# Kernel optimization log

Measured on AMD Instinct MI355X. Metric: run time of the kernel, lower is better.

## Reference

```python
import jax, jax.numpy as jnp
import numpy as np

T, B, E, H = 2048, 2, 1024, 16
D = E // H
MAX_REL = 16  # RelativePosition default max_relative_position


def setup_inputs() -> dict:
    key = jax.random.key(0)
    ks = jax.random.split(key, 11)
    s = 1.0 / np.sqrt(E)
    inp = {
        'query': jax.random.normal(ks[0], (T, B, E), dtype=jnp.float32),
        'Wq': jax.random.normal(ks[1], (E, E), dtype=jnp.float32) * s,
        'bq': jnp.zeros((E,), dtype=jnp.float32),
        'Wk': jax.random.normal(ks[2], (E, E), dtype=jnp.float32) * s,
        'bk': jnp.zeros((E,), dtype=jnp.float32),
        'Wv': jax.random.normal(ks[3], (E, E), dtype=jnp.float32) * s,
        'bv': jnp.zeros((E,), dtype=jnp.float32),
        'Wo': jax.random.normal(ks[4], (E, E), dtype=jnp.float32) * s,
        'bo': jnp.zeros((E,), dtype=jnp.float32),
        'rk_table': jax.random.normal(ks[5], (2 * MAX_REL + 1, D), dtype=jnp.float32) * 0.05,
        'rv_table': jax.random.normal(ks[6], (2 * MAX_REL + 1, D), dtype=jnp.float32) * 0.05,
    }
    return inp


def _rel_idx(lq, lk):
    # distance_mat = k - q, clipped to [-MAX_REL, MAX_REL], shifted to [0, 2*MAX_REL]
    d = jnp.arange(lk)[None, :] - jnp.arange(lq)[:, None]
    return jnp.clip(d, -MAX_REL, MAX_REL) + MAX_REL  # [lq, lk] int


def reference(query, Wq, bq, Wk, bk, Wv, bv, Wo, bo, rk_table, rv_table):
    t, b, e = query.shape
    scale = D ** -0.5
    # projections (torch Linear: x @ W.T + b)
    q = (query @ Wq.T + bq) * scale
    k = query @ Wk.T + bk
    v = query @ Wv.T + bv
    # [T,B,E] -> [B*H, T, D]
    q = q.reshape(t, b * H, D).transpose(1, 0, 2)
    k = k.reshape(t, b * H, D).transpose(1, 0, 2)
    v = v.reshape(t, b * H, D).transpose(1, 0, 2)
    # content scores + Shaw relative-position key scores
    scores = jnp.einsum('ntd,nsd->nts', q, k)            # [N, T, S]
    rk = rk_table[_rel_idx(t, t)]                        # [T, S, D]
    scores = scores + jnp.einsum('ntd,tsd->nts', q, rk)  # relpos_k term
    probs = jax.nn.softmax(scores, axis=-1)
    # weighted values + Shaw relative-position value term
    rv = rv_table[_rel_idx(t, t)]                        # [T, S, D]
    attn = jnp.einsum('nts,nsd->ntd', probs, v) + jnp.einsum('nts,tsd->ntd', probs, rv)
    # [B*H, T, D] -> [T, B, E]
    attn = attn.transpose(1, 0, 2).reshape(t, b, e)
    return attn @ Wo.T + bo
```

## Files before the change

kernel.cpp:

```cpp
#include <hip/hip_runtime.h>
#include <hip/hip_bf16.h>
#include <math.h>

#define T_   2048
#define B_   2
#define E_   1024
#define H_   16
#define D_   64
#define NH_  32
#define M_   4096

typedef __attribute__((ext_vector_type(8))) short s8b;
typedef __attribute__((ext_vector_type(4))) float f4;

#define MFMA_B16(a,b,c) __builtin_amdgcn_mfma_f32_16x16x32_bf16(a,b,c,0,0,0)
#define LOG2E 1.44269504088896f

__device__ __forceinline__ unsigned short f2bu(float f) {
    union { __hip_bfloat16 h; unsigned short u; } cv;
    cv.h = __float2bfloat16(f);
    return cv.u;
}
__device__ __forceinline__ unsigned short f2bu_fast(float f) {
    return (unsigned short)((__float_as_uint(f) + 0x8000u) >> 16);
}
__device__ __forceinline__ float bu2f(unsigned short u) {
    union { __hip_bfloat16 h; unsigned short u; } cv; cv.u = u;
    return __bfloat162float(cv.h);
}
__device__ __forceinline__ unsigned int pk2(float a, float b) {
    return (unsigned int)f2bu(a) | ((unsigned int)f2bu(b) << 16);
}
__device__ __forceinline__ unsigned int pk2_fast(float a, float b) {
    return ((__float_as_uint(a) + 0x8000u) >> 16) |
           ((__float_as_uint(b) + 0x8000u) & 0xFFFF0000u);
}
__device__ __forceinline__ float fexp2(float x) {
    return __builtin_amdgcn_exp2f(x);
}
__device__ __forceinline__ float ld1d(const void* p, size_t idx, bool f32) {
    return f32 ? ((const float*)p)[idx] : bu2f(((const unsigned short*)p)[idx]);
}
__device__ __forceinline__ float qsumq(float v) {
    v += __shfl_xor(v, 16); v += __shfl_xor(v, 32);
    return v;
}
__device__ __forceinline__ void glds16(const unsigned short* g, unsigned short* l) {
    __builtin_amdgcn_global_load_lds(
        (const __attribute__((address_space(1))) unsigned int*)g,
        (__attribute__((address_space(3))) unsigned int*)l, 16, 0, 0);
}

__global__ void detect_dtype(const unsigned short* __restrict__ q, int* __restrict__ flag) {
    int e = (q[threadIdx.x] >> 7) & 0xFF;
    bool sane = (e == 0) || (e >= 97 && e <= 157);
    unsigned long long m = __ballot(sane);
    if (threadIdx.x == 0) *flag = (__popcll(m) >= 56) ? 0 : 1;
}

__global__ __launch_bounds__(256) void cvt_bf16(
    const void* __restrict__ x,
    const void* __restrict__ Wq, const void* __restrict__ Wk,
    const void* __restrict__ Wv, const void* __restrict__ Wo,
    const void* __restrict__ bq, const void* __restrict__ bk,
    const void* __restrict__ bv, const void* __restrict__ bo,
    unsigned short* __restrict__ xw, unsigned short* __restrict__ Ww,
    unsigned short* __restrict__ bw, const int* __restrict__ flag)
{
    const bool f32m = (*flag != 0);
    const int y = blockIdx.y;
    const void* src; unsigned short* dst; int n;
    if (y == 0)      { src = x; dst = xw; n = M_ * E_; }
    else if (y <= 4) {
        src = (y == 1) ? Wq : (y == 2) ? Wk : (y == 3) ? Wv : Wo;
        dst = Ww + (size_t)(y - 1) * E_ * E_; n = E_ * E_;
    } else {
        src = (y == 5) ? bq : (y == 6) ? bk : (y == 7) ? bv : bo;
        dst = bw + (size_t)(y - 5) * E_; n = E_;
    }
    int i = (blockIdx.x * 256 + threadIdx.x) * 8;
    if (i >= n) return;
    if (f32m) {
        const float* s = (const float*)src + i;
        float4 f0 = *(const float4*)s, f1 = *(const float4*)(s + 4);
        union { unsigned int d[4]; s8b v; } u;
        u.d[0] = pk2(f0.x, f0.y); u.d[1] = pk2(f0.z, f0.w);
        u.d[2] = pk2(f1.x, f1.y); u.d[3] = pk2(f1.z, f1.w);
        *(s8b*)(dst + i) = u.v;
    } else {
        *(s8b*)(dst + i) = *(const s8b*)((const unsigned short*)src + i);
    }
}

__global__ __launch_bounds__(256, 3) void qkv_gemm(
    const unsigned short* __restrict__ xw, const unsigned short* __restrict__ Ww,
    const unsigned short* __restrict__ bw,
    unsigned short* __restrict__ qo, unsigned short* __restrict__ ko,
    unsigned short* __restrict__ vo)
{
    const int bid = blockIdx.x;
    const int r_ = bid & 7, s_ = bid >> 3;
    const int g = r_ + 8 * (s_ >> 3);
    const int e0 = (s_ & 7) * 128;
    const int m0 = (g & 31) * 128;
    const int p  = g >> 5;
    const unsigned short* W    = Ww + (size_t)p * E_ * E_;
    const unsigned short* bias = bw + (size_t)p * E_;
    const float scale = (p == 0) ? 0.125f * LOG2E : 1.0f;

    const int tid = threadIdx.x, w = tid >> 6, lane = tid & 63;
    const int quad = lane >> 4, lc = lane & 15;
    const int wx = w & 1, wy = w >> 1;

    __shared__ unsigned short a_s[2][128 * 32];
    __shared__ unsigned short b_s[2][128 * 32];

    f4 acc[4][4];
    #pragma unroll
    for (int i = 0; i < 4; i++)
        #pragma unroll
        for (int j = 0; j < 4; j++) acc[i][j] = (f4){0.f, 0.f, 0.f, 0.f};

    const int gr = lane >> 2;
    const int gc = (lane & 3) ^ ((lane >> 2) & 3);
    const size_t aoff = (size_t)(m0 + w*32 + gr) * E_ + gc*8;
    const size_t boff = (size_t)(e0 + w*32 + gr) * E_ + gc*8;

    #pragma unroll
    for (int j = 0; j < 2; j++) {
        glds16(xw + aoff + (size_t)j*16*E_, &a_s[0][(w*128 + j*64) * 8]);
        glds16(W  + boff + (size_t)j*16*E_, &b_s[0][(w*128 + j*64) * 8]);
    }
    __syncthreads();

    const int fcA = quad ^ (lc & 3);
    for (int k0 = 0; k0 < E_; k0 += 32) {
        const int cur = (k0 >> 5) & 1;
        if (k0 + 32 < E_) {
            #pragma unroll
            for (int j = 0; j < 2; j++) {
                glds16(xw + aoff + (size_t)j*16*E_ + k0 + 32, &a_s[cur^1][(w*128 + j*64) * 8]);
                glds16(W  + boff + (size_t)j*16*E_ + k0 + 32, &b_s[cur^1][(w*128 + j*64) * 8]);
            }
        }
        s8b af[4], bfr[4];
        #pragma unroll
        for (int i = 0; i < 4; i++)
            af[i]  = *(const s8b*)&a_s[cur][((wy*64 + i*16 + lc)*4 + fcA) * 8];
        #pragma unroll
        for (int i = 0; i < 4; i++)
            bfr[i] = *(const s8b*)&b_s[cur][((wx*64 + i*16 + lc)*4 + fcA) * 8];
        #pragma unroll
        for (int ms = 0; ms < 4; ms++)
            #pragma unroll
            for (int ns = 0; ns < 4; ns++)
                acc[ms][ns] = MFMA_B16(af[ms], bfr[ns], acc[ms][ns]);
        __syncthreads();
    }

    float bias_v[4];
    #pragma unroll
    for (int ns = 0; ns < 4; ns++) bias_v[ns] = bu2f(bias[e0 + wx*64 + ns*16 + lc]);

    if (p < 2) {
        #pragma unroll
        for (int ms = 0; ms < 4; ms++)
            #pragma unroll
            for (int ns = 0; ns < 4; ns++)
                #pragma unroll
                for (int r2 = 0; r2 < 4; r2++) {
                    float val = (acc[ms][ns][r2] + bias_v[ns]) * scale;
                    float nb = __shfl_xor(val, 1);
                    if (!(lane & 1)) {
                        int m = m0 + wy*64 + ms*16 + quad*4 + r2;
                        int t = m >> 1, bb = m & 1;
                        int e = e0 + wx*64 + ns*16 + lc;
                        int h = e >> 6, d = e & 63;
                        unsigned short* dst = (p == 0) ? qo : ko;
                        *(unsigned int*)&dst[(((size_t)(bb*H_ + h) * T_ + t) << 6) + d] = pk2(val, nb);
                    }
                }
    } else {
        #pragma unroll
        for (int ms = 0; ms < 4; ms++) {
            int t0v = (m0 + wy*64 + ms*16 + quad*4) >> 1;
            #pragma unroll
            for (int ns = 0; ns < 4; ns++) {
                int e = e0 + wx*64 + ns*16 + lc;
                int h = e >> 6, d = e & 63;
                float v0 = acc[ms][ns][0] + bias_v[ns];
                float v1 = acc[ms][ns][1] + bias_v[ns];
                float v2 = acc[ms][ns][2] + bias_v[ns];
                float v3 = acc[ms][ns][3] + bias_v[ns];
                *(unsigned int*)&vo[((size_t)h        * 64 + d) * T_ + t0v] = pk2(v0, v2);
                *(unsigned int*)&vo[((size_t)(H_ + h) * 64 + d) * T_ + t0v] = pk2(v1, v3);
            }
        }
    }
}

__global__ __launch_bounds__(256, 2) void attn_mfma(
    const unsigned short* __restrict__ q, const unsigned short* __restrict__ k,
    const unsigned short* __restrict__ v,
    const void* __restrict__ rk_t, const void* __restrict__ rv_t,
    unsigned short* __restrict__ aout, const int* __restrict__ flag)
{
    const bool f32m = (*flag != 0);
    const int bid = blockIdx.x;
    const int n = bid & 31, qt = bid >> 5;
    const int t0 = qt * 128;
    const int tid = threadIdx.x, w = tid >> 6, lane = tid & 63;
    const int quad = lane >> 4, lc = lane & 15;

    __shared__ unsigned short k_s[2][64 * 64];
    __shared__ unsigned short v_s[2][64 * 64];
    __shared__ unsigned short p_s[4][32 * 72];
    __shared__ unsigned short qrk_s[128 * 36];
    __shared__ unsigned short diag16[128 * 33];
    __shared__ float st_L[128], st_R[128];

    const unsigned short* qn = q + ((size_t)n * T_ + t0) * D_;
    const unsigned short* kn = k + (size_t)n * T_ * D_;
    const unsigned short* vn = v + (size_t)n * D_ * T_;

    s8b qa[2][2];
    #pragma unroll
    for (int nt = 0; nt < 2; nt++)
        #pragma unroll
        for (int kf = 0; kf < 2; kf++)
            qa[nt][kf] = *(const s8b*)(qn + (size_t)(w*32 + nt*16 + lc) * D_ + kf*32 + quad*8);

    for (int i = tid; i < 128 * 33; i += 256) diag16[i] = 0;

    unsigned int* rks = (unsigned int*)&p_s[0][0];
    for (int i = tid; i < 48 * 36; i += 256) {
        int r = i / 36, c2 = i % 36;
        unsigned int val = 0;
        if (r < 33 && c2 < 32)
            val = pk2(ld1d(rk_t, r*64 + 2*c2, f32m), ld1d(rk_t, r*64 + 2*c2 + 1, f32m));
        rks[i] = val;
    }
    __syncthreads();

    #pragma unroll
    for (int mt = 0; mt < 2; mt++)
        for (int nt = 0; nt < 3; nt++) {
            s8b b0 = *(const s8b*)((const unsigned short*)rks + (nt*16 + lc)*72 + quad*8);
            s8b b1 = *(const s8b*)((const unsigned short*)rks + (nt*16 + lc)*72 + 32 + quad*8);
            f4 a = (f4){0.f, 0.f, 0.f, 0.f};
            a = MFMA_B16(qa[mt][0], b0, a);
            a = MFMA_B16(qa[mt][1], b1, a);
            #pragma unroll
            for (int r = 0; r < 4; r++) {
                float nb = __shfl_xor(a[r], 1);
                int col = nt*16 + lc;
                if (!(lane & 1) && col < 34)
                    ((unsigned int*)qrk_s)[(w*32 + mt*16 + quad*4 + r)*18 + (col >> 1)] = pk2(a[r], nb);
            }
        }
    __syncthreads();

    float qLn[2], qRn[2];
    float L_p[2] = {0.f, 0.f}, R_p[2] = {0.f, 0.f};
    f4 O[4][2], lsN[2], lsL[2], lsR[2];
    #pragma unroll
    for (int nt = 0; nt < 2; nt++) {
        int row = w*32 + nt*16 + lc;
        qLn[nt] = bu2f(qrk_s[row*36 + 0]);
        qRn[nt] = bu2f(qrk_s[row*36 + 32]);
        lsN[nt] = (f4){0.f, 0.f, 0.f, 0.f};
        lsL[nt] = (f4){0.f, 0.f, 0.f, 0.f};
        lsR[nt] = (f4){0.f, 0.f, 0.f, 0.f};
        #pragma unroll
        for (int dt = 0; dt < 4; dt++) O[dt][nt] = (f4){0.f, 0.f, 0.f, 0.f};
    }
    const short ob = (short)0x3F80;
    const s8b ones = { ob, ob, ob, ob, ob, ob, ob, ob };

    const int grr = lane >> 3;
    const int gcc = (lane & 7) ^ grr;
    const size_t koff = (size_t)(w*16 + grr) * D_ + gcc*8;
    const size_t voff = (size_t)(w*16 + grr) * T_ + gcc*8;

    s8b kr0 = *(const s8b*)(kn + koff);
    s8b kr1 = *(const s8b*)(kn + koff + 8*D_);
    s8b vr0 = *(const s8b*)(vn + voff);
    s8b vr1 = *(const s8b*)(vn + voff + (size_t)8*T_);
    *(s8b*)&k_s[0][(w*128 +      lane) * 8] = kr0;
    *(s8b*)&k_s[0][(w*128 + 64 + lane) * 8] = kr1;
    *(s8b*)&v_s[0][(w*128 +      lane) * 8] = vr0;
    *(s8b*)&v_s[0][(w*128 + 64 + lane) * 8] = vr1;
    __syncthreads();

    const int lc7 = lc & 7;
    for (int kt = 0; kt < 32; kt++) {
        const int s0 = kt * 64;
        const int cur = kt & 1;
        if (kt + 1 < 32) {
            kr0 = *(const s8b*)(kn + koff + (size_t)(s0 + 64)*D_);
            kr1 = *(const s8b*)(kn + koff + (size_t)(s0 + 72)*D_);
            vr0 = *(const s8b*)(vn + voff + s0 + 64);
            vr1 = *(const s8b*)(vn + voff + (size_t)8*T_ + s0 + 64);
        }

        const bool farL  = (s0 + 63 < t0 - 16);
        const bool farR  = (s0 > t0 + 143);
        const bool nearT = !farL && !farR;

        s8b ak[4][2];
        #pragma unroll
        for (int st = 0; st < 4; st++) {
            int row = st*16 + lc;
            ak[st][0] = *(const s8b*)&k_s[cur][(row*8 + (quad       ^ lc7)) * 8];
            ak[st][1] = *(const s8b*)&k_s[cur][(row*8 + ((4 + quad) ^ lc7)) * 8];
        }

        #pragma unroll
        for (int st = 0; st < 4; st++)
            #pragma unroll
            for (int nt = 0; nt < 2; nt++) {
                f4 a;
                if (nearT) a = (f4){0.f, 0.f, 0.f, 0.f};
                else {
                    float qb = farL ? qLn[nt] : qRn[nt];
                    a = (f4){qb, qb, qb, qb};
                }
                a = MFMA_B16(ak[st][0], qa[nt][0], a);
                a = MFMA_B16(ak[st][1], qa[nt][1], a);
                unsigned int lo, hi;
                if (nearT) {
                    const int t_l = w*32 + nt*16 + lc;
                    const int sb  = s0 + st*16 + quad*4 - (t0 + t_l);
                    unsigned short eb[4];
                    #pragma unroll
                    for (int r = 0; r < 4; r++) {
                        int rel = sb + r;
                        int rc = rel < -16 ? -16 : (rel > 16 ? 16 : rel);
                        float e = fexp2(a[r] + bu2f(qrk_s[t_l*36 + rc + 16]));
                        eb[r] = f2bu_fast(e);
                        if (rel <= -16)      L_p[nt] += e;
                        else if (rel >= 16)  R_p[nt] += e;
                        else                 diag16[t_l*33 + rel + 15] = eb[r];
                    }
                    lo = (unsigned int)eb[0] | ((unsigned int)eb[1] << 16);
                    hi = (unsigned int)eb[2] | ((unsigned int)eb[3] << 16);
                } else {
                    lo = pk2_fast(fexp2(a[0]), fexp2(a[1]));
                    hi = pk2_fast(fexp2(a[2]), fexp2(a[3]));
                }
                *(uint2*)&p_s[w][(nt*16 + lc)*72 + st*16 + quad*4] = make_uint2(lo, hi);
            }

        s8b pb[2][2];
        #pragma unroll
        for (int nt = 0; nt < 2; nt++) {
            pb[nt][0] = *(const s8b*)&p_s[w][(nt*16 + lc)*72 + quad*8];
            pb[nt][1] = *(const s8b*)&p_s[w][(nt*16 + lc)*72 + 32 + quad*8];
        }
        if (nearT) {
            #pragma unroll
            for (int nt = 0; nt < 2; nt++) {
                lsN[nt] = MFMA_B16(ones, pb[nt][0], lsN[nt]);
                lsN[nt] = MFMA_B16(ones, pb[nt][1], lsN[nt]);
            }
        } else if (farL) {
            #pragma unroll
            for (int nt = 0; nt < 2; nt++) {
                lsL[nt] = MFMA_B16(ones, pb[nt][0], lsL[nt]);
                lsL[nt] = MFMA_B16(ones, pb[nt][1], lsL[nt]);
            }
        } else {
            #pragma unroll
            for (int nt = 0; nt < 2; nt++) {
                lsR[nt] = MFMA_B16(ones, pb[nt][0], lsR[nt]);
                lsR[nt] = MFMA_B16(ones, pb[nt][1], lsR[nt]);
            }
        }
        #pragma unroll
        for (int dt = 0; dt < 4; dt++) {
            int row = dt*16 + lc;
            s8b a0 = *(const s8b*)&v_s[cur][(row*8 + (quad       ^ lc7)) * 8];
            s8b a1 = *(const s8b*)&v_s[cur][(row*8 + ((4 + quad) ^ lc7)) * 8];
            O[dt][0] = MFMA_B16(a0, pb[0][0], O[dt][0]);
            O[dt][0] = MFMA_B16(a1, pb[0][1], O[dt][0]);
            O[dt][1] = MFMA_B16(a0, pb[1][0], O[dt][1]);
            O[dt][1] = MFMA_B16(a1, pb[1][1], O[dt][1]);
        }

        if (kt + 1 < 32) {
            *(s8b*)&k_s[cur ^ 1][(w*128 +      lane) * 8] = kr0;
            *(s8b*)&k_s[cur ^ 1][(w*128 + 64 + lane) * 8] = kr1;
            *(s8b*)&v_s[cur ^ 1][(w*128 +      lane) * 8] = vr0;
            *(s8b*)&v_s[cur ^ 1][(w*128 + 64 + lane) * 8] = vr1;
        }
        __syncthreads();
    }

    float linv[2];
    #pragma unroll
    for (int nt = 0; nt < 2; nt++) {
        float l = lsN[nt][0] + lsL[nt][0] + lsR[nt][0];
        float L = lsL[nt][0] + qsumq(L_p[nt]);
        float R = lsR[nt][0] + qsumq(R_p[nt]);
        linv[nt] = 1.f / l;
        if (quad == 0) {
            int row = w*32 + nt*16 + lc;
            st_L[row] = L; st_R[row] = R;
        }
    }
    {
        unsigned int* rvs = (unsigned int*)&k_s[0][0];
        for (int i = tid; i < 64 * 32; i += 256) {
            int d = i >> 5, dwL = i & 31;
            int r0 = dwL * 2, r1 = r0 + 1;
            float x0 = (r0 < 33) ? ld1d(rv_t, (size_t)r0 * 64 + d, f32m) : 0.f;
            float x1 = (r1 < 33) ? ld1d(rv_t, (size_t)r1 * 64 + d, f32m) : 0.f;
            int phys = d * 32 + ((dwL >> 2) ^ (d & 7)) * 4 + (dwL & 3);
            rvs[phys] = pk2(x0, x1);
        }
    }
    __syncthreads();
    for (int j = 0; j < 32; j++) {
        int c = lane;
        int row = w*32 + j;
        unsigned short pv;
        if (c == 0)        pv = f2bu(st_L[row]);
        else if (c == 32)  pv = f2bu(st_R[row]);
        else if (c < 32)   pv = diag16[row*33 + c - 1];
        else               pv = 0;
        p_s[w][j*72 + c] = pv;
    }
    s8b pe[2][2];
    #pragma unroll
    for (int nt = 0; nt < 2; nt++) {
        pe[nt][0] = *(const s8b*)&p_s[w][(nt*16 + lc)*72 + quad*8];
        pe[nt][1] = *(const s8b*)&p_s[w][(nt*16 + lc)*72 + 32 + quad*8];
    }
    #pragma unroll
    for (int dt = 0; dt < 4; dt++) {
        int row = dt*16 + lc;
        s8b a0 = *(const s8b*)&k_s[0][(row*8 + (quad       ^ lc7)) * 8];
        s8b a1 = *(const s8b*)&k_s[0][(row*8 + ((4 + quad) ^ lc7)) * 8];
        O[dt][0] = MFMA_B16(a0, pe[0][0], O[dt][0]);
        O[dt][0] = MFMA_B16(a1, pe[0][1], O[dt][0]);
        O[dt][1] = MFMA_B16(a0, pe[1][0], O[dt][1]);
        O[dt][1] = MFMA_B16(a1, pe[1][1], O[dt][1]);
    }
    const int bb = n >> 4, h = n & 15;
    #pragma unroll
    for (int nt = 0; nt < 2; nt++) {
        int t_g = t0 + w*32 + nt*16 + lc;
        #pragma unroll
        for (int dt = 0; dt < 4; dt++) {
            float v0 = O[dt][nt][0] * linv[nt];
            float v1 = O[dt][nt][1] * linv[nt];
            float v2 = O[dt][nt][2] * linv[nt];
            float v3 = O[dt][nt][3] * linv[nt];
            int e = h*64 + dt*16 + quad*4;
            *(uint2*)&aout[((size_t)t_g * B_ + bb) * E_ + e] =
                make_uint2(pk2(v0, v1), pk2(v2, v3));
        }
    }
}

__global__ __launch_bounds__(256, 3) void out_gemm(
    const unsigned short* __restrict__ A,
    const unsigned short* __restrict__ Wob, const unsigned short* __restrict__ bob,
    void* __restrict__ out, const int* __restrict__ flag)
{
    const bool f32m = (*flag != 0);
    const int bid = blockIdx.x;
    const int r_ = bid & 7, s_ = bid >> 3;
    const int g = r_ + 8 * (s_ >> 3);
    const int m0 = g * 128;
    const int e0 = (s_ & 7) * 128;

    const int tid = threadIdx.x, w = tid >> 6, lane = tid & 63;
    const int quad = lane >> 4, lc = lane & 15;
    const int wx = w & 1, wy = w >> 1;

    __shared__ unsigned short a_s[2][128 * 32];
    __shared__ unsigned short b_s[2][128 * 32];

    f4 acc[4][4];
    #pragma unroll
    for (int i = 0; i < 4; i++)
        #pragma unroll
        for (int j = 0; j < 4; j++) acc[i][j] = (f4){0.f, 0.f, 0.f, 0.f};

    const int gr = lane >> 2;
    const int gc = (lane & 3) ^ ((lane >> 2) & 3);
    const size_t aoff = (size_t)(m0 + w*32 + gr) * E_ + gc*8;
    const size_t boff = (size_t)(e0 + w*32 + gr) * E_ + gc*8;

    #pragma unroll
    for (int j = 0; j < 2; j++) {
        glds16(A   + aoff + (size_t)j*16*E_, &a_s[0][(w*128 + j*64) * 8]);
        glds16(Wob + boff + (size_t)j*16*E_, &b_s[0][(w*128 + j*64) * 8]);
    }
    __syncthreads();

    const int fcA = quad ^ (lc & 3);
    for (int k0 = 0; k0 < E_; k0 += 32) {
        const int cur = (k0 >> 5) & 1;
        if (k0 + 32 < E_) {
            #pragma unroll
            for (int j = 0; j < 2; j++) {
                glds16(A   + aoff + (size_t)j*16*E_ + k0 + 32, &a_s[cur^1][(w*128 + j*64) * 8]);
                glds16(Wob + boff + (size_t)j*16*E_ + k0 + 32, &b_s[cur^1][(w*128 + j*64) * 8]);
            }
        }
        s8b af[4], bfr[4];
        #pragma unroll
        for (int i = 0; i < 4; i++)
            af[i]  = *(const s8b*)&a_s[cur][((wy*64 + i*16 + lc)*4 + fcA) * 8];
        #pragma unroll
        for (int i = 0; i < 4; i++)
            bfr[i] = *(const s8b*)&b_s[cur][((wx*64 + i*16 + lc)*4 + fcA) * 8];
        #pragma unroll
        for (int ms = 0; ms < 4; ms++)
            #pragma unroll
            for (int ns = 0; ns < 4; ns++)
                acc[ms][ns] = MFMA_B16(af[ms], bfr[ns], acc[ms][ns]);
        __syncthreads();
    }

    float bias_v[4];
    #pragma unroll
    for (int ns = 0; ns < 4; ns++) bias_v[ns] = bu2f(bob[e0 + wx*64 + ns*16 + lc]);

    #pragma unroll
    for (int ms = 0; ms < 4; ms++)
        #pragma unroll
        for (int ns = 0; ns < 4; ns++)
            #pragma unroll
            for (int r2 = 0; r2 < 4; r2++) {
                float val = acc[ms][ns][r2] + bias_v[ns];
                size_t m = m0 + wy*64 + ms*16 + quad*4 + r2;
                int e = e0 + wx*64 + ns*16 + lc;
                if (f32m) {
                    ((float*)out)[m * E_ + e] = val;
                } else {
                    float nb = __shfl_xor(val, 1);
                    if (!(lane & 1))
                        *(unsigned int*)&((unsigned short*)out)[m * E_ + e] = pk2(val, nb);
                }
            }
}

extern "C" void kernel_launch(void* const* d_in, const int* in_sizes, int n_in,
                              void* d_out, int out_size, void* d_ws, size_t ws_size,
                              hipStream_t stream) {
    const void* x  = d_in[0];
    const void* Wq = d_in[1];  const void* bq = d_in[2];
    const void* Wk = d_in[3];  const void* bk = d_in[4];
    const void* Wv = d_in[5];  const void* bv = d_in[6];
    const void* Wo = d_in[7];  const void* bo = d_in[8];
    const void* rk = d_in[9];  const void* rv = d_in[10];

    int* flag = (int*)d_ws;
    const size_t HTD = (size_t)NH_ * T_ * D_;
    unsigned short* qw = (unsigned short*)((char*)d_ws + 256);
    unsigned short* kw = qw + HTD;
    unsigned short* vw = kw + HTD;
    unsigned short* aw = vw + HTD;
    unsigned short* xw = aw + (size_t)M_ * E_;
    unsigned short* Ww = xw + (size_t)M_ * E_;
    unsigned short* bw = Ww + (size_t)4 * E_ * E_;

    detect_dtype<<<1, 64, 0, stream>>>((const unsigned short*)x, flag);
    cvt_bf16<<<dim3((M_*E_/8 + 255)/256, 9), 256, 0, stream>>>(
        x, Wq, Wk, Wv, Wo, bq, bk, bv, bo, xw, Ww, bw, flag);
    qkv_gemm<<<dim3(768), 256, 0, stream>>>(xw, Ww, bw, qw, kw, vw);
    attn_mfma<<<dim3(NH_ * (T_/128)), 256, 0, stream>>>(qw, kw, vw, rk, rv, aw, flag);
    out_gemm<<<dim3(256), 256, 0, stream>>>(aw, Ww + (size_t)3*E_*E_, bw + 3*E_,
                                            d_out, flag);
}
```

Measured before the change: 235.5 us.

## Single-buffer K/V shared tiles and raise attention occupancy to three blocks

Replaces the double-buffered K and V LDS tiles with single buffers and adds an extra barrier before overwriting them each iteration. The launch bound rises from 2 to 3 blocks per CU so the lower LDS and register budget lets more waves hide latency. In exchange, each key tile now costs two barriers, and the tighter register cap may cause spills in a kernel that keeps many MFMA accumulators live.

After: 239.5 us. No clear change (+1.7%).

```diff
diff --git a/kernel.cpp b/kernel.cpp
--- a/kernel.cpp
+++ b/kernel.cpp
@@ -199,7 +199,7 @@
     }
 }
 
-__global__ __launch_bounds__(256, 2) void attn_mfma(
+__global__ __launch_bounds__(256, 3) void attn_mfma(
     const unsigned short* __restrict__ q, const unsigned short* __restrict__ k,
     const unsigned short* __restrict__ v,
     const void* __restrict__ rk_t, const void* __restrict__ rv_t,
@@ -212,8 +212,8 @@
     const int tid = threadIdx.x, w = tid >> 6, lane = tid & 63;
     const int quad = lane >> 4, lc = lane & 15;
 
-    __shared__ unsigned short k_s[2][64 * 64];
-    __shared__ unsigned short v_s[2][64 * 64];
+    __shared__ unsigned short k_s[64 * 64];
+    __shared__ unsigned short v_s[64 * 64];
     __shared__ unsigned short p_s[4][32 * 72];
     __shared__ unsigned short qrk_s[128 * 36];
     __shared__ unsigned short diag16[128 * 33];
@@ -286,16 +286,15 @@
     s8b kr1 = *(const s8b*)(kn + koff + 8*D_);
     s8b vr0 = *(const s8b*)(vn + voff);
     s8b vr1 = *(const s8b*)(vn + voff + (size_t)8*T_);
-    *(s8b*)&k_s[0][(w*128 +      lane) * 8] = kr0;
-    *(s8b*)&k_s[0][(w*128 + 64 + lane) * 8] = kr1;
-    *(s8b*)&v_s[0][(w*128 +      lane) * 8] = vr0;
-    *(s8b*)&v_s[0][(w*128 + 64 + lane) * 8] = vr1;
+    *(s8b*)&k_s[(w*128 +      lane) * 8] = kr0;
+    *(s8b*)&k_s[(w*128 + 64 + lane) * 8] = kr1;
+    *(s8b*)&v_s[(w*128 +      lane) * 8] = vr0;
+    *(s8b*)&v_s[(w*128 + 64 + lane) * 8] = vr1;
     __syncthreads();
 
     const int lc7 = lc & 7;
     for (int kt = 0; kt < 32; kt++) {
         const int s0 = kt * 64;
-        const int cur = kt & 1;
         if (kt + 1 < 32) {
             kr0 = *(const s8b*)(kn + koff + (size_t)(s0 + 64)*D_);
             kr1 = *(const s8b*)(kn + koff + (size_t)(s0 + 72)*D_);
@@ -311,8 +310,8 @@
         #pragma unroll
         for (int st = 0; st < 4; st++) {
             int row = st*16 + lc;
-            ak[st][0] = *(const s8b*)&k_s[cur][(row*8 + (quad       ^ lc7)) * 8];
-            ak[st][1] = *(const s8b*)&k_s[cur][(row*8 + ((4 + quad) ^ lc7)) * 8];
+            ak[st][0] = *(const s8b*)&k_s[(row*8 + (quad       ^ lc7)) * 8];
+            ak[st][1] = *(const s8b*)&k_s[(row*8 + ((4 + quad) ^ lc7)) * 8];
         }
 
         #pragma unroll
@@ -379,19 +378,20 @@
         #pragma unroll
         for (int dt = 0; dt < 4; dt++) {
             int row = dt*16 + lc;
-            s8b a0 = *(const s8b*)&v_s[cur][(row*8 + (quad       ^ lc7)) * 8];
-            s8b a1 = *(const s8b*)&v_s[cur][(row*8 + ((4 + quad) ^ lc7)) * 8];
+            s8b a0 = *(const s8b*)&v_s[(row*8 + (quad       ^ lc7)) * 8];
+            s8b a1 = *(const s8b*)&v_s[(row*8 + ((4 + quad) ^ lc7)) * 8];
             O[dt][0] = MFMA_B16(a0, pb[0][0], O[dt][0]);
             O[dt][0] = MFMA_B16(a1, pb[0][1], O[dt][0]);
             O[dt][1] = MFMA_B16(a0, pb[1][0], O[dt][1]);
             O[dt][1] = MFMA_B16(a1, pb[1][1], O[dt][1]);
         }
 
+        __syncthreads();
         if (kt + 1 < 32) {
-            *(s8b*)&k_s[cur ^ 1][(w*128 +      lane) * 8] = kr0;
-            *(s8b*)&k_s[cur ^ 1][(w*128 + 64 + lane) * 8] = kr1;
-            *(s8b*)&v_s[cur ^ 1][(w*128 +      lane) * 8] = vr0;
-            *(s8b*)&v_s[cur ^ 1][(w*128 + 64 + lane) * 8] = vr1;
+            *(s8b*)&k_s[(w*128 +      lane) * 8] = kr0;
+            *(s8b*)&k_s[(w*128 + 64 + lane) * 8] = kr1;
+            *(s8b*)&v_s[(w*128 +      lane) * 8] = vr0;
+            *(s8b*)&v_s[(w*128 + 64 + lane) * 8] = vr1;
         }
         __syncthreads();
     }
@@ -409,7 +409,7 @@
         }
     }
     {
-        unsigned int* rvs = (unsigned int*)&k_s[0][0];
+        unsigned int* rvs = (unsigned int*)&k_s[0];
         for (int i = tid; i < 64 * 32; i += 256) {
             int d = i >> 5, dwL = i & 31;
             int r0 = dwL * 2, r1 = r0 + 1;
@@ -439,8 +439,8 @@
     #pragma unroll
     for (int dt = 0; dt < 4; dt++) {
         int row = dt*16 + lc;
-        s8b a0 = *(const s8b*)&k_s[0][(row*8 + (quad       ^ lc7)) * 8];
-        s8b a1 = *(const s8b*)&k_s[0][(row*8 + ((4 + quad) ^ lc7)) * 8];
+        s8b a0 = *(const s8b*)&k_s[(row*8 + (quad       ^ lc7)) * 8];
+        s8b a1 = *(const s8b*)&k_s[(row*8 + ((4 + quad) ^ lc7)) * 8];
         O[dt][0] = MFMA_B16(a0, pe[0][0], O[dt][0]);
         O[dt][0] = MFMA_B16(a1, pe[0][1], O[dt][0]);
         O[dt][1] = MFMA_B16(a0, pe[1][0], O[dt][1]);
```
